# Kernel tuning notes

Hardware: AMD Instinct MI355X
Metric: run time of the kernel (lower is better)

## Reference

```python
import jax, jax.numpy as jnp
import numpy as np

N_GRAPHS = 256
NODES_PER_GRAPH = 64
N_NODES = N_GRAPHS * NODES_PER_GRAPH  # 16384
IN_F = 128
OUT_F = 128
N_HEADS = 16


def setup_inputs() -> dict:
    key = jax.random.key(0)
    k1, k2, k3, k4 = jax.random.split(key, 4)
    inputs = jax.random.normal(k1, (N_NODES, IN_F), dtype=jnp.float32)
    # fixed equal-sized graphs so sum(n_node) == N_NODES exactly
    n_node = jnp.full((N_GRAPHS,), NODES_PER_GRAPH, dtype=jnp.int32)
    head = jax.random.randint(k2, (N_GRAPHS,), 0, N_HEADS, dtype=jnp.int32)
    # lecun_normal-like init: std = 1/sqrt(fan_in)
    kernel = jax.random.normal(k3, (N_HEADS, IN_F, OUT_F), dtype=jnp.float32) * (1.0 / np.sqrt(IN_F))
    bias = jax.random.normal(k4, (N_HEADS, OUT_F), dtype=jnp.float32) * 0.02
    return {"inputs": inputs, "n_node": n_node, "head": head, "kernel": kernel, "bias": bias}


def reference(inputs, n_node, head, kernel, bias):
    # per-node head index: repeat each graph's head over its nodes
    node_head = jnp.repeat(head, n_node, total_repeat_length=inputs.shape[0])  # [N]
    k = kernel[node_head]                       # [N, in, out] (gathered per-node weights)
    y = jnp.einsum('bi,bio->bo', inputs, k)     # [N, out]
    y = y + bias[node_head]                     # [N, out]
    return y
```

## Files before the change

### kernel.cpp

```cpp
#include <hip/hip_runtime.h>
#include <hip/hip_bf16.h>

#define NG   256
#define NPG  64
#define INF  128
#define OUTF 128
#define NH   16

typedef __attribute__((ext_vector_type(8))) short bf16x8;
typedef __attribute__((ext_vector_type(4))) float f32x4;

__device__ __forceinline__ ushort f2bf(float f) {
    union { float f; unsigned int i; } c; c.f = f;
    unsigned int r = c.i + 0x7fffu + ((c.i >> 16) & 1u);
    return (ushort)(r >> 16);
}

__global__ __launch_bounds__(256) void transpose_w_kernel(
    const float* __restrict__ W, ushort* __restrict__ Wt)
{
    int h  = blockIdx.x >> 2;
    int k0 = ((blockIdx.x >> 1) & 1) * 64;
    int n0 = (blockIdx.x & 1) * 64;
    int t  = (int)threadIdx.x;
    int n  = t & 63;
    int kg = t >> 6;

    const float* src = W + h * (INF * OUTF) + (k0 + kg * 16) * OUTF + (n0 + n);
    ushort vals[16] __attribute__((aligned(16)));
#pragma unroll
    for (int j = 0; j < 16; ++j) vals[j] = f2bf(src[j * OUTF]);

    ushort* dst = Wt + h * (INF * OUTF) + (n0 + n) * INF + (k0 + kg * 16);
    *(uint4*)(dst)     = *(const uint4*)(&vals[0]);
    *(uint4*)(dst + 8) = *(const uint4*)(&vals[8]);
}

__global__ __launch_bounds__(512) void mhl_gemm_kernel(
    const float*  __restrict__ X,
    const int*    __restrict__ head,
    const ushort* __restrict__ Wt,
    const float*  __restrict__ bias,
    float*        __restrict__ Y)
{
    int g    = (int)blockIdx.x;
    int h    = head[g];
    int wave = (int)threadIdx.x >> 6;
    int lane = (int)threadIdx.x & 63;
    int quad = lane >> 4;
    int l16  = lane & 15;

    int mrow = (wave & 3) * 16;
    int ncol = (wave >> 2) * 64;

    const float* Xg = X + (g * NPG + mrow + l16) * INF + quad * 8;
    bf16x8 a[4];
#pragma unroll
    for (int kt = 0; kt < 4; ++kt) {
        float v[8] __attribute__((aligned(16)));
        *(float4*)(&v[0]) = *(const float4*)(Xg + kt * 32);
        *(float4*)(&v[4]) = *(const float4*)(Xg + kt * 32 + 4);
#pragma unroll
        for (int j = 0; j < 8; ++j) a[kt][j] = (short)f2bf(v[j]);
    }

    const ushort* Wh = Wt + h * (INF * OUTF);
    f32x4 acc[4];
#pragma unroll
    for (int nt = 0; nt < 4; ++nt) acc[nt] = (f32x4){0.f, 0.f, 0.f, 0.f};

#pragma unroll
    for (int nt = 0; nt < 4; ++nt) {
        const ushort* Wn = Wh + (ncol + nt * 16 + l16) * INF + quad * 8;
#pragma unroll
        for (int kt = 0; kt < 4; ++kt) {
            bf16x8 b = *(const bf16x8*)(Wn + kt * 32);
            acc[nt] = __builtin_amdgcn_mfma_f32_16x16x32_bf16(a[kt], b, acc[nt], 0, 0, 0);
        }
    }

    float* Yg = Y + (g * NPG + mrow) * OUTF + ncol;
#pragma unroll
    for (int nt = 0; nt < 4; ++nt) {
        float bv = bias[h * OUTF + ncol + nt * 16 + l16];
#pragma unroll
        for (int r = 0; r < 4; ++r)
            Yg[(quad * 4 + r) * OUTF + nt * 16 + l16] = acc[nt][r] + bv;
    }
}

extern "C" void kernel_launch(void* const* d_in, const int* in_sizes, int n_in,
                              void* d_out, int out_size, void* d_ws, size_t ws_size,
                              hipStream_t stream) {
    const float* X    = (const float*)d_in[0];
    const int*   head = (const int*)d_in[2];
    const float* W    = (const float*)d_in[3];
    const float* bias = (const float*)d_in[4];
    float*  Y  = (float*)d_out;
    ushort* Wt = (ushort*)d_ws;

    transpose_w_kernel<<<NH * 4, 256, 0, stream>>>(W, Wt);
    mhl_gemm_kernel<<<NG, 512, 0, stream>>>(X, head, Wt, bias, Y);
}
```

Measured before the change: 75.54 us.

## Fuse weight transpose into GEMM kernel via per-block LDS staging

Removes the separate transpose/convert kernel and its workspace round trip. Each block now loads its head's fp32 weight matrix, converts it to bf16 and writes it transposed into padded shared memory, then runs the MFMA GEMM reading B from LDS. This drops one kernel launch and the dependency between the two kernels. In exchange every one of the 256 blocks re-reads and re-converts a 64KB fp32 weight slice instead of 16 heads doing it once, and the scalar 2-byte strided LDS stores may cause bank conflicts.

```diff
diff --git a/kernel.cpp b/kernel.cpp
--- a/kernel.cpp
+++ b/kernel.cpp
@@ -6,6 +6,8 @@
 #define INF  128
 #define OUTF 128
 #define NH   16
+
+#define LDSK 136
 
 typedef __attribute__((ext_vector_type(8))) short bf16x8;
 typedef __attribute__((ext_vector_type(4))) float f32x4;
@@ -16,37 +18,36 @@
     return (ushort)(r >> 16);
 }
 
-__global__ __launch_bounds__(256) void transpose_w_kernel(
-    const float* __restrict__ W, ushort* __restrict__ Wt)
+__global__ __launch_bounds__(512) void mhl_fused_kernel(
+    const float* __restrict__ X,
+    const int*   __restrict__ head,
+    const float* __restrict__ W,
+    const float* __restrict__ bias,
+    float*       __restrict__ Y)
 {
-    int h  = blockIdx.x >> 2;
-    int k0 = ((blockIdx.x >> 1) & 1) * 64;
-    int n0 = (blockIdx.x & 1) * 64;
-    int t  = (int)threadIdx.x;
-    int n  = t & 63;
-    int kg = t >> 6;
+    __shared__ ushort Wl[OUTF * LDSK];
 
-    const float* src = W + h * (INF * OUTF) + (k0 + kg * 16) * OUTF + (n0 + n);
-    ushort vals[16] __attribute__((aligned(16)));
+    int g = (int)blockIdx.x;
+    int h = head[g];
+    int t = (int)threadIdx.x;
+
+    {
+        int k  = t >> 2;
+        int c0 = (t & 3) * 32;
+        const float* src = W + h * (INF * OUTF) + k * OUTF + c0;
 #pragma unroll
-    for (int j = 0; j < 16; ++j) vals[j] = f2bf(src[j * OUTF]);
+        for (int j = 0; j < 32; j += 4) {
+            float4 v = *(const float4*)(src + j);
+            Wl[(c0 + j + 0) * LDSK + k] = f2bf(v.x);
+            Wl[(c0 + j + 1) * LDSK + k] = f2bf(v.y);
+            Wl[(c0 + j + 2) * LDSK + k] = f2bf(v.z);
+            Wl[(c0 + j + 3) * LDSK + k] = f2bf(v.w);
+        }
+    }
+    __syncthreads();
 
-    ushort* dst = Wt + h * (INF * OUTF) + (n0 + n) * INF + (k0 + kg * 16);
-    *(uint4*)(dst)     = *(const uint4*)(&vals[0]);
-    *(uint4*)(dst + 8) = *(const uint4*)(&vals[8]);
-}
-
-__global__ __launch_bounds__(512) void mhl_gemm_kernel(
-    const float*  __restrict__ X,
-    const int*    __restrict__ head,
-    const ushort* __restrict__ Wt,
-    const float*  __restrict__ bias,
-    float*        __restrict__ Y)
-{
-    int g    = (int)blockIdx.x;
-    int h    = head[g];
-    int wave = (int)threadIdx.x >> 6;
-    int lane = (int)threadIdx.x & 63;
+    int wave = t >> 6;
+    int lane = t & 63;
     int quad = lane >> 4;
     int l16  = lane & 15;
 
@@ -64,14 +65,13 @@
         for (int j = 0; j < 8; ++j) a[kt][j] = (short)f2bf(v[j]);
     }
 
-    const ushort* Wh = Wt + h * (INF * OUTF);
     f32x4 acc[4];
 #pragma unroll
     for (int nt = 0; nt < 4; ++nt) acc[nt] = (f32x4){0.f, 0.f, 0.f, 0.f};
 
 #pragma unroll
     for (int nt = 0; nt < 4; ++nt) {
-        const ushort* Wn = Wh + (ncol + nt * 16 + l16) * INF + quad * 8;
+        const ushort* Wn = &Wl[(ncol + nt * 16 + l16) * LDSK + quad * 8];
 #pragma unroll
         for (int kt = 0; kt < 4; ++kt) {
             bf16x8 b = *(const bf16x8*)(Wn + kt * 32);
@@ -96,9 +96,7 @@
     const int*   head = (const int*)d_in[2];
     const float* W    = (const float*)d_in[3];
     const float* bias = (const float*)d_in[4];
-    float*  Y  = (float*)d_out;
-    ushort* Wt = (ushort*)d_ws;
+    float* Y = (float*)d_out;
 
-    transpose_w_kernel<<<NH * 4, 256, 0, stream>>>(W, Wt);
-    mhl_gemm_kernel<<<NG, 512, 0, stream>>>(X, head, Wt, bias, Y);
+    mhl_fused_kernel<<<NG, 512, 0, stream>>>(X, head, W, bias, Y);
 }
```

New measurement: 72.06 us. -4.6%, faster.
